# Optimization experiments

Hardware: AMD Instinct MI355X
Metric: run time of the kernel (lower is better)

## Reference

```python
import jax, jax.numpy as jnp
import numpy as np

B, N, L, H, D, IN = 512, 128, 10, 16, 8, 16
NT = B * N
E = NT * 16

def _lin(key, fan_in, shape):
    b = 1.0 / np.sqrt(fan_in)
    return jax.random.uniform(key, shape, jnp.float32, -b, b)

def setup_inputs() -> dict:
    key = jax.random.key(0)
    ks = jax.random.split(key, 12)
    x = jax.random.normal(ks[0], (NT, IN), jnp.float32)
    # within-graph random edges so to_dense_adj is well defined
    g = jax.random.randint(ks[1], (E,), 0, B)
    i = jax.random.randint(ks[2], (E,), 0, N)
    j = jax.random.randint(ks[3], (E,), 0, N)
    edge_index = jnp.stack([g * N + i, g * N + j]).astype(jnp.int32)
    return dict(
        x=x,
        gin_w1=_lin(ks[4], H, (2, L, H, H)),   # [ld/ud, layer, H, H]
        gin_b1=_lin(ks[5], H, (2, L, H)),
        gin_w2=_lin(ks[6], H, (2, L, H, H)),
        gin_b2=_lin(ks[7], H, (2, L, H)),
        mean_w=_lin(ks[8], H, (2, H, D)),
        mean_b=jnp.zeros((2, D), jnp.float32),
        std_w=_lin(ks[9], H, (2, H, D)),
        std_b=jnp.zeros((2, D), jnp.float32),
        edge_index=edge_index,
    )

def _encoder(x, w1, b1, w2, b2, mw, mb, sw, sb, src, dst):
    # PyG GIN stack: GINConv(MLP[Lin->ReLU->Lin]), eps=0, sum aggregation,
    # ReLU between layers (dropout = identity in eval mode).
    h = x
    for l in range(L):
        agg = jax.ops.segment_sum(h[src], dst, num_segments=NT)
        t = h + agg  # (1+eps)*x + sum_{j in N(i)} x_j with eps=0
        t = jnp.maximum(t @ w1[l] + b1[l], 0.0) @ w2[l] + b2[l]
        h = jnp.maximum(t, 0.0) if l < L - 1 else t
    mean = h @ mw + mb
    std = jax.nn.softplus(h @ sw + sb)
    return mean, std

def reference(x, gin_w1, gin_b1, gin_w2, gin_b2, mean_w, mean_b, std_w, std_b, edge_index):
    src, dst = edge_index[0], edge_index[1]
    enc = jax.vmap(_encoder, in_axes=(None, 0, 0, 0, 0, 0, 0, 0, 0, None, None))
    mean, std = enc(x, gin_w1, gin_b1, gin_w2, gin_b2,
                    mean_w, mean_b, std_w, std_b, src, dst)  # [2, NT, D]
    # reparameterized sample: eps ~ N(0,1) (prior.sample, detached)
    eps = jax.random.normal(jax.random.key(42), (2, NT, D), jnp.float32)
    z = mean + std * eps
    z_ld = z[0].reshape(B, N, D)
    z_ud = z[1].reshape(B, N, D)
    logits = jnp.einsum('bnd,bmd->bnm', z_ld, z_ud)  # per-graph inner-product decode
    dense_adj = jnp.zeros((B, N, N), jnp.float32).at[src // N, src % N, dst % N].add(1.0)
    n_pos = dense_adj.sum()
    posw = (B * N * N - n_pos) / n_pos
    # BCE-with-logits, pos_weight, reduction='sum'
    nll = jnp.sum(posw * dense_adj * jax.nn.softplus(-logits)
                  + (1.0 - dense_adj) * jax.nn.softplus(logits))
    # KL(N(mean,std) || N(0,1)), summed over both encoders
    kl = jnp.sum(-jnp.log(std) + 0.5 * (std * std + mean * mean) - 0.5)
    return nll, kl, jax.nn.sigmoid(logits), dense_adj
```

## Files before the change

kernel.cpp:

```cpp
#include <hip/hip_runtime.h>

#define B_    512
#define N_    128
#define L_    10
#define H_    16
#define D_    8
#define NT_   65536
#define E_    1048576
#define NNB_  8388608
#define CAP_  4096
#define CCAP_ 2816
#define HS_   20

__device__ __forceinline__ unsigned rotl32(unsigned v, int r){ return (v<<r)|(v>>(32-r)); }

__device__ __forceinline__ void threefry2x32(unsigned c0, unsigned c1, unsigned &o0, unsigned &o1){
  const unsigned ks0 = 0u, ks1 = 42u, ks2 = 0u ^ 42u ^ 0x1BD11BDAu;
  unsigned x0 = c0 + ks0, x1 = c1 + ks1;
#define TFR(r) { x0 += x1; x1 = rotl32(x1, r); x1 ^= x0; }
  TFR(13) TFR(15) TFR(26) TFR(6)   x0 += ks1; x1 += ks2 + 1u;
  TFR(17) TFR(29) TFR(16) TFR(24)  x0 += ks2; x1 += ks0 + 2u;
  TFR(13) TFR(15) TFR(26) TFR(6)   x0 += ks0; x1 += ks1 + 3u;
  TFR(17) TFR(29) TFR(16) TFR(24)  x0 += ks1; x1 += ks2 + 4u;
  TFR(13) TFR(15) TFR(26) TFR(6)   x0 += ks2; x1 += ks0 + 5u;
#undef TFR
  o0 = x0; o1 = x1;
}

__device__ __forceinline__ float erfinv_f(float x){
  float w = -log1pf(-x*x);
  float p;
  if (w < 5.0f) {
    w -= 2.5f;
    p = 2.81022636e-08f;
    p = fmaf(p, w, 3.43273939e-07f);
    p = fmaf(p, w, -3.5233877e-06f);
    p = fmaf(p, w, -4.39150654e-06f);
    p = fmaf(p, w, 0.00021858087f);
    p = fmaf(p, w, -0.00125372503f);
    p = fmaf(p, w, -0.00417768164f);
    p = fmaf(p, w, 0.246640727f);
    p = fmaf(p, w, 1.50140941f);
  } else {
    w = sqrtf(w) - 3.0f;
    p = -0.000200214257f;
    p = fmaf(p, w, 0.000100950558f);
    p = fmaf(p, w, 0.00134934322f);
    p = fmaf(p, w, -0.00367342844f);
    p = fmaf(p, w, 0.00573950773f);
    p = fmaf(p, w, -0.0076224613f);
    p = fmaf(p, w, 0.00943887047f);
    p = fmaf(p, w, 1.00167406f);
    p = fmaf(p, w, 2.83297682f);
  }
  return p * x;
}

__device__ __forceinline__ float softplus_f(float x){
  return fmaxf(x, 0.0f) + log1pf(expf(-fabsf(x)));
}

__device__ __forceinline__ void blockReduceAdd(double v, double* target){
  __shared__ double red[4];
  int lane = threadIdx.x & 63;
  int w    = threadIdx.x >> 6;
  #pragma unroll
  for(int off = 32; off > 0; off >>= 1) v += __shfl_down(v, off);
  if(lane == 0) red[w] = v;
  __syncthreads();
  if(threadIdx.x == 0){
    double s = red[0];
    int nw = (blockDim.x + 63) >> 6;
    for(int k = 1; k < nw; k++) s += red[k];
    atomicAdd(target, s);
  }
}

__global__ __launch_bounds__(256)
void k_bin(const int* __restrict__ ei, int* __restrict__ gcount,
           unsigned short* __restrict__ ebuf){
  __shared__ int cnt[512];
  __shared__ int gb[512];
  const int t = threadIdx.x;
  cnt[t] = 0; cnt[t + 256] = 0;
  __syncthreads();
  int kv[8];
  const int base = blockIdx.x * 2048;
  #pragma unroll
  for(int q = 0; q < 8; q++){
    int e = base + q*256 + t;
    int s = ei[e];
    int d = ei[E_ + e];
    int g = d >> 7;
    kv[q] = (g << 14) | ((s & 127) << 7) | (d & 127);
    atomicAdd(&cnt[g], 1);
  }
  __syncthreads();
  #pragma unroll
  for(int g = 0; g < 512; g += 256){
    int c = cnt[g + t];
    gb[g + t] = c ? atomicAdd(&gcount[g + t], c) : 0;
    cnt[g + t] = 0;
  }
  __syncthreads();
  #pragma unroll
  for(int q = 0; q < 8; q++){
    int g = kv[q] >> 14;
    int pos = atomicAdd(&cnt[g], 1);
    int idx = gb[g] + pos;
    if(idx < CAP_) ebuf[(size_t)g*CAP_ + idx] = (unsigned short)(kv[q] & 0x3FFF);
  }
}

__global__ __launch_bounds__(128)
void k_csr(const unsigned short* __restrict__ ebuf, const int* __restrict__ gcount,
           unsigned short* __restrict__ gcol, int* __restrict__ grow){
  __shared__ int cnt[128], off[128], sc[128];
  const int b = blockIdx.x, t = threadIdx.x;
  int ec = gcount[b]; if(ec > CAP_) ec = CAP_;
  const unsigned short* eb = ebuf + (size_t)b*CAP_;
  cnt[t] = 0;
  __syncthreads();
  for(int q = t; q < ec; q += 128) atomicAdd(&cnt[eb[q] & 127], 1);
  __syncthreads();
  int pdeg = (cnt[t] + 3) & ~3;
  sc[t] = pdeg;
  __syncthreads();
  for(int o = 1; o < 128; o <<= 1){
    int v = (t >= o) ? sc[t - o] : 0;
    __syncthreads();
    sc[t] += v;
    __syncthreads();
  }
  off[t] = sc[t] - pdeg;
  grow[b*129 + t] = off[t];
  if(t == 127) grow[b*129 + 128] = sc[127];
  cnt[t] = 0;
  __syncthreads();
  {
    uint4 s128; s128.x = s128.y = s128.z = s128.w = 0x00800080u;
    uint4* g4 = (uint4*)(gcol + (size_t)b*CCAP_);
    #pragma unroll
    for(int k = 0; k < 3; k++){ int q = t + 128*k; if(q < CCAP_/8) g4[q] = s128; }
  }
  __syncthreads();
  for(int q = t; q < ec; q += 128){
    int pk = eb[q];
    int d = pk & 127;
    int pos = atomicAdd(&cnt[d], 1);
    int idx = off[d] + pos;
    if(idx < CCAP_) gcol[(size_t)b*CCAP_ + idx] = (unsigned short)(pk >> 7);
  }
}

__global__ __launch_bounds__(128, 4)
void k_mega(const float* __restrict__ x, const unsigned short* __restrict__ gcol,
            const int* __restrict__ grow,
            const float* __restrict__ gw1, const float* __restrict__ gb1,
            const float* __restrict__ gw2, const float* __restrict__ gb2,
            const float* __restrict__ mw,  const float* __restrict__ mb,
            const float* __restrict__ sw,  const float* __restrict__ sb,
            float* __restrict__ z, double* acc){
  __shared__ __align__(16) float hh[129*HS_ + 4];
  __shared__ __align__(16) unsigned short col_l[CCAP_];
  const int b = blockIdx.x, e = blockIdx.y, t = threadIdx.x;

  {
    const float4* x4 = (const float4*)x + (size_t)b*512;
    #pragma unroll
    for(int k = 0; k < 4; k++){
      int q = t + 128*k;
      float4 v = x4[q];
      *(float4*)&hh[(q >> 2)*HS_ + (q & 3)*4] = v;
    }
    if(t < 16) hh[128*HS_ + t] = 0.0f;
  }
  {
    const uint4* gc4 = (const uint4*)(gcol + (size_t)b*CCAP_);
    uint4* cl4 = (uint4*)col_l;
    #pragma unroll
    for(int k = 0; k < 3; k++){ int q = t + 128*k; if(q < CCAP_/8) cl4[q] = gc4[q]; }
  }
  const int r0 = grow[b*129 + t], r1 = grow[b*129 + t + 1];
  __syncthreads();

  const float* w1g = gw1 + e*(L_*256);
  const float* w2g = gw2 + e*(L_*256);
  const float* b1g = gb1 + e*(L_*16);
  const float* b2g = gb2 + e*(L_*16);

  for(int l = 0; l < L_; l++){
    float ag[16];
    {
      const float4* hp = (const float4*)&hh[t*HS_];
      float4 s0 = hp[0], s1 = hp[1], s2 = hp[2], s3 = hp[3];
      ag[0]=s0.x; ag[1]=s0.y; ag[2]=s0.z; ag[3]=s0.w;
      ag[4]=s1.x; ag[5]=s1.y; ag[6]=s1.z; ag[7]=s1.w;
      ag[8]=s2.x; ag[9]=s2.y; ag[10]=s2.z; ag[11]=s2.w;
      ag[12]=s3.x; ag[13]=s3.y; ag[14]=s3.z; ag[15]=s3.w;
    }
    for(int r = r0; r < r1; r += 4){
      ushort4 c4 = *(const ushort4*)&col_l[r];
      const float4* n0 = (const float4*)&hh[c4.x*HS_];
      const float4* n1 = (const float4*)&hh[c4.y*HS_];
      const float4* n2 = (const float4*)&hh[c4.z*HS_];
      const float4* n3 = (const float4*)&hh[c4.w*HS_];
      #pragma unroll
      for(int c = 0; c < 4; c++){
        float4 v0 = n0[c], v1 = n1[c], v2 = n2[c], v3 = n3[c];
        ag[c*4+0] += v0.x + v1.x + v2.x + v3.x;
        ag[c*4+1] += v0.y + v1.y + v2.y + v3.y;
        ag[c*4+2] += v0.z + v1.z + v2.z + v3.z;
        ag[c*4+3] += v0.w + v1.w + v2.w + v3.w;
      }
    }
    float u[16];
    #pragma unroll
    for(int j = 0; j < 16; j++){
      float s = b1g[l*16 + j];
      #pragma unroll
      for(int k = 0; k < 16; k++) s = fmaf(ag[k], w1g[l*256 + k*16 + j], s);
      u[j] = fmaxf(s, 0.0f);
    }
    float ov[16];
    #pragma unroll
    for(int c = 0; c < 16; c++){
      float s = b2g[l*16 + c];
      #pragma unroll
      for(int k = 0; k < 16; k++) s = fmaf(u[k], w2g[l*256 + k*16 + c], s);
      ov[c] = (l < L_-1) ? fmaxf(s, 0.0f) : s;
    }
    __syncthreads();
    {
      float4* hw = (float4*)&hh[t*HS_];
      hw[0] = make_float4(ov[0], ov[1], ov[2], ov[3]);
      hw[1] = make_float4(ov[4], ov[5], ov[6], ov[7]);
      hw[2] = make_float4(ov[8], ov[9], ov[10], ov[11]);
      hw[3] = make_float4(ov[12], ov[13], ov[14], ov[15]);
    }
    __syncthreads();
  }

  float hv[16];
  {
    const float4* hp = (const float4*)&hh[t*HS_];
    float4 a0 = hp[0], a1 = hp[1], a2 = hp[2], a3 = hp[3];
    hv[0]=a0.x; hv[1]=a0.y; hv[2]=a0.z; hv[3]=a0.w;
    hv[4]=a1.x; hv[5]=a1.y; hv[6]=a1.z; hv[7]=a1.w;
    hv[8]=a2.x; hv[9]=a2.y; hv[10]=a2.z; hv[11]=a2.w;
    hv[12]=a3.x; hv[13]=a3.y; hv[14]=a3.z; hv[15]=a3.w;
  }
  const float* mwg = mw + e*128; const float* mbg = mb + e*8;
  const float* swg = sw + e*128; const float* sbg = sb + e*8;
  double kll = 0.0;
  float zv[8];
  unsigned fbase = ((unsigned)e*NT_ + (unsigned)(b*128 + t))*8u;
  #pragma unroll
  for(int d = 0; d < 8; d++){
    float mm = mbg[d], ss = sbg[d];
    #pragma unroll
    for(int k = 0; k < 16; k++){
      mm = fmaf(hv[k], mwg[k*8 + d], mm);
      ss = fmaf(hv[k], swg[k*8 + d], ss);
    }
    float stdv = softplus_f(ss);
    unsigned o0, o1; threefry2x32(0u, fbase + d, o0, o1);
    unsigned bits = o0 ^ o1;
    float uu = __uint_as_float((bits >> 9) | 0x3f800000u) - 1.0f;
    const float lo = -0.99999994f;
    float uval = fmaxf(lo, fmaf(uu, 2.0f, lo));
    float eps = 1.41421356f * erfinv_f(uval);
    zv[d] = mm + stdv * eps;
    float stdc = fmaxf(stdv, 1e-37f);
    float term = 0.5f*(stdv*stdv + mm*mm) - logf(stdc) - 0.5f;
    if(!(term == term) || term > 1e30f) term = 1e30f;
    kll += (double)term;
  }
  {
    float4* zp = (float4*)(z + (size_t)fbase);
    zp[0] = make_float4(zv[0], zv[1], zv[2], zv[3]);
    zp[1] = make_float4(zv[4], zv[5], zv[6], zv[7]);
  }
  blockReduceAdd(kll, acc + 1);
}

#define TSB_ 132
__global__ __launch_bounds__(256, 4)
void k_decode(const float* __restrict__ z, const unsigned short* __restrict__ ebuf,
              const int* __restrict__ gcount, float* __restrict__ sig,
              float* __restrict__ adj, double* acc){
  __shared__ float zl[1024];
  __shared__ float zu[1152];
  __shared__ unsigned tile32[128*TSB_/4];
  const int b = blockIdx.x, t = threadIdx.x;
  const float* zld = z + (size_t)b*1024;
  const float* zud = z + (size_t)NT_*8 + (size_t)b*1024;
  for(int k = t; k < 1024; k += 256){
    zl[k] = zld[k];
    zu[(k >> 3)*9 + (k & 7)] = zud[k];
  }
  {
    uint4 zz; zz.x = zz.y = zz.z = zz.w = 0u;
    uint4* t4 = (uint4*)tile32;
    for(int k = t; k < 128*TSB_/16; k += 256) t4[k] = zz;
  }
  __syncthreads();
  {
    int ec = gcount[b]; if(ec > CAP_) ec = CAP_;
    const unsigned short* eb = ebuf + (size_t)b*CAP_;
    for(int q = t; q < ec; q += 256){
      int pk = eb[q];
      int cell = (pk >> 7)*TSB_ + (pk & 127);
      atomicAdd(&tile32[cell >> 2], 1u << ((cell & 3)*8));
    }
  }
  __syncthreads();
  double local = 0.0;
  float* sigb = sig + (size_t)b*16384;
  float* adjb = adj + (size_t)b*16384;
  for(int it = 0; it < 16; it++){
    int base = it*1024 + t*4;
    int n = base >> 7, mcol = base & 127;
    const float* za = &zl[n*8];
    float xs[4];
    #pragma unroll
    for(int c = 0; c < 4; c++){
      const float* zb = &zu[(mcol + c)*9];
      float xx = 0.0f;
      #pragma unroll
      for(int d = 0; d < 8; d++) xx = fmaf(za[d], zb[d], xx);
      xs[c] = xx;
    }
    unsigned packed = tile32[(n*TSB_ + mcol) >> 2];
    float4 av;
    av.x = (float)( packed        & 0xFF);
    av.y = (float)((packed >> 8)  & 0xFF);
    av.z = (float)((packed >> 16) & 0xFF);
    av.w = (float)((packed >> 24) & 0xFF);
    float ads[4] = {av.x, av.y, av.z, av.w};
    float sgs[4];
    #pragma unroll
    for(int c = 0; c < 4; c++){
      float xx = xs[c];
      sgs[c] = 1.0f / (1.0f + expf(-xx));
      float cc  = log1pf(expf(-fabsf(xx)));
      float spp = fmaxf(xx, 0.0f) + cc;
      float spn = fmaxf(-xx, 0.0f) + cc;
      local += (double)(7.0f*ads[c]*spn + (1.0f - ads[c])*spp);
    }
    ((float4*)(sigb + base))[0] = make_float4(sgs[0], sgs[1], sgs[2], sgs[3]);
    ((float4*)(adjb + base))[0] = av;
  }
  blockReduceAdd(local, acc + 0);
}

__device__ __forceinline__ float clamp_finite(double v){
  if(v != v) return 0.0f;
  if(v >  3.3e38) return  3.3e38f;
  if(v < -3.3e38) return -3.3e38f;
  return (float)v;
}
__global__ void k_final(const double* __restrict__ acc, float* __restrict__ out){
  if(threadIdx.x == 0){
    out[0] = clamp_finite(acc[0]);
    out[1] = clamp_finite(acc[1]);
  }
}

extern "C" void kernel_launch(void* const* d_in, const int* in_sizes, int n_in,
                              void* d_out, int out_size, void* d_ws, size_t ws_size,
                              hipStream_t stream){
  const float* x   = (const float*)d_in[0];
  const float* gw1 = (const float*)d_in[1];
  const float* gb1 = (const float*)d_in[2];
  const float* gw2 = (const float*)d_in[3];
  const float* gb2 = (const float*)d_in[4];
  const float* mw  = (const float*)d_in[5];
  const float* mb  = (const float*)d_in[6];
  const float* sw  = (const float*)d_in[7];
  const float* sb  = (const float*)d_in[8];
  const int*   ei  = (const int*)d_in[9];

  float* out = (float*)d_out;
  float* sig = out + 2;
  float* adj = out + 2 + NNB_;

  char* ws = (char*)d_ws;
  int*            gcount = (int*)(ws);
  double*         acc    = (double*)(ws + 2048);
  unsigned short* ebuf   = (unsigned short*)(ws + 4096);
  unsigned short* gcol   = (unsigned short*)(ws + 4096 + 2*512*CAP_);
  int*            grow   = (int*)(ws + 4096 + 2*512*CAP_ + 2*512*CCAP_);
  float*          z      = (float*)(ws + 4096 + 2*512*CAP_ + 2*512*CCAP_ + 4*512*132);

  hipMemsetAsync(ws, 0, 4096, stream);

  k_bin   <<<E_/2048, 256, 0, stream>>>(ei, gcount, ebuf);
  k_csr   <<<B_, 128, 0, stream>>>(ebuf, gcount, gcol, grow);
  k_mega  <<<dim3(B_, 2), 128, 0, stream>>>(x, gcol, grow, gw1, gb1, gw2, gb2,
                                            mw, mb, sw, sb, z, acc);
  k_decode<<<B_, 256, 0, stream>>>(z, ebuf, gcount, sig, adj, acc);
  k_final <<<1, 64, 0, stream>>>(acc, out);
}
```

Measured before the change: 236.5 us.

## Fuse CSR build into GIN kernel and split features across 4 threads per node

Removes the separate k_csr kernel and builds the per-graph CSR directly in shared memory inside k_mega, which drops one launch and the global round trip through gcol/grow. k_mega now runs 512 threads per block, with four threads per node. Each thread handles a quarter of the hidden features for aggregation and the MLPs, exchanging them through new shared buffers agg_l and u_l. The aim is more parallelism and latency hiding per graph. The cost is extra barriers and shared-memory traffic per layer, and the CSR build is now done twice, once for each encoder block.

After: 233.6 us. No clear change (-1.2%).

```diff
diff --git a/kernel.cpp b/kernel.cpp
--- a/kernel.cpp
+++ b/kernel.cpp
@@ -61,7 +61,7 @@
 }
 
 __device__ __forceinline__ void blockReduceAdd(double v, double* target){
-  __shared__ double red[4];
+  __shared__ double red[8];
   int lane = threadIdx.x & 63;
   int w    = threadIdx.x >> 6;
   #pragma unroll
@@ -112,77 +112,68 @@
   }
 }
 
-__global__ __launch_bounds__(128)
-void k_csr(const unsigned short* __restrict__ ebuf, const int* __restrict__ gcount,
-           unsigned short* __restrict__ gcol, int* __restrict__ grow){
-  __shared__ int cnt[128], off[128], sc[128];
-  const int b = blockIdx.x, t = threadIdx.x;
-  int ec = gcount[b]; if(ec > CAP_) ec = CAP_;
-  const unsigned short* eb = ebuf + (size_t)b*CAP_;
-  cnt[t] = 0;
-  __syncthreads();
-  for(int q = t; q < ec; q += 128) atomicAdd(&cnt[eb[q] & 127], 1);
-  __syncthreads();
-  int pdeg = (cnt[t] + 3) & ~3;
-  sc[t] = pdeg;
-  __syncthreads();
-  for(int o = 1; o < 128; o <<= 1){
-    int v = (t >= o) ? sc[t - o] : 0;
-    __syncthreads();
-    sc[t] += v;
-    __syncthreads();
-  }
-  off[t] = sc[t] - pdeg;
-  grow[b*129 + t] = off[t];
-  if(t == 127) grow[b*129 + 128] = sc[127];
-  cnt[t] = 0;
-  __syncthreads();
-  {
-    uint4 s128; s128.x = s128.y = s128.z = s128.w = 0x00800080u;
-    uint4* g4 = (uint4*)(gcol + (size_t)b*CCAP_);
-    #pragma unroll
-    for(int k = 0; k < 3; k++){ int q = t + 128*k; if(q < CCAP_/8) g4[q] = s128; }
-  }
-  __syncthreads();
-  for(int q = t; q < ec; q += 128){
-    int pk = eb[q];
-    int d = pk & 127;
-    int pos = atomicAdd(&cnt[d], 1);
-    int idx = off[d] + pos;
-    if(idx < CCAP_) gcol[(size_t)b*CCAP_ + idx] = (unsigned short)(pk >> 7);
-  }
-}
-
-__global__ __launch_bounds__(128, 4)
-void k_mega(const float* __restrict__ x, const unsigned short* __restrict__ gcol,
-            const int* __restrict__ grow,
+__global__ __launch_bounds__(512, 8)
+void k_mega(const float* __restrict__ x, const unsigned short* __restrict__ ebuf,
+            const int* __restrict__ gcount,
             const float* __restrict__ gw1, const float* __restrict__ gb1,
             const float* __restrict__ gw2, const float* __restrict__ gb2,
             const float* __restrict__ mw,  const float* __restrict__ mb,
             const float* __restrict__ sw,  const float* __restrict__ sb,
             float* __restrict__ z, double* acc){
   __shared__ __align__(16) float hh[129*HS_ + 4];
+  __shared__ __align__(16) float agg_l[128*HS_];
+  __shared__ __align__(16) float u_l[128*HS_];
   __shared__ __align__(16) unsigned short col_l[CCAP_];
+  __shared__ int cnt[128];
+  __shared__ int sc[128];
+  __shared__ int off_l[129];
+
   const int b = blockIdx.x, e = blockIdx.y, t = threadIdx.x;
+  const int lane = t & 63;
+  const int q  = __builtin_amdgcn_readfirstlane((t >> 6) & 3);
+  const int q4 = q * 4;
+  const int n  = lane + ((t >> 8) << 6);
 
   {
     const float4* x4 = (const float4*)x + (size_t)b*512;
-    #pragma unroll
-    for(int k = 0; k < 4; k++){
-      int q = t + 128*k;
-      float4 v = x4[q];
-      *(float4*)&hh[(q >> 2)*HS_ + (q & 3)*4] = v;
-    }
+    float4 v = x4[t];
+    *(float4*)&hh[(t >> 2)*HS_ + (t & 3)*4] = v;
     if(t < 16) hh[128*HS_ + t] = 0.0f;
-  }
+    if(t < 128) cnt[t] = 0;
+  }
+  __syncthreads();
+
+  int ec = gcount[b]; if(ec > CAP_) ec = CAP_;
+  const unsigned short* eb = ebuf + (size_t)b*CAP_;
+  for(int i = t; i < ec; i += 512) atomicAdd(&cnt[eb[i] & 127], 1);
+  __syncthreads();
+  int pdeg = 0;
+  if(t < 128){ pdeg = (cnt[t] + 3) & ~3; sc[t] = pdeg; }
+  __syncthreads();
+  for(int o = 1; o < 128; o <<= 1){
+    int v = 0;
+    if(t < 128 && t >= o) v = sc[t - o];
+    __syncthreads();
+    if(t < 128) sc[t] += v;
+    __syncthreads();
+  }
+  if(t < 128){ off_l[t] = sc[t] - pdeg; cnt[t] = 0; }
+  if(t == 127) off_l[128] = sc[127];
   {
-    const uint4* gc4 = (const uint4*)(gcol + (size_t)b*CCAP_);
-    uint4* cl4 = (uint4*)col_l;
-    #pragma unroll
-    for(int k = 0; k < 3; k++){ int q = t + 128*k; if(q < CCAP_/8) cl4[q] = gc4[q]; }
-  }
-  const int r0 = grow[b*129 + t], r1 = grow[b*129 + t + 1];
-  __syncthreads();
+    uint4 s128; s128.x = s128.y = s128.z = s128.w = 0x00800080u;
+    uint4* c4 = (uint4*)col_l;
+    if(t < CCAP_/8) c4[t] = s128;
+  }
+  __syncthreads();
+  for(int i = t; i < ec; i += 512){
+    int pk = eb[i];
+    int d = pk & 127;
+    int pos = atomicAdd(&cnt[d], 1);
+    int idx = off_l[d] + pos;
+    if(idx < CCAP_) col_l[idx] = (unsigned short)(pk >> 7);
+  }
+  __syncthreads();
+  const int r0 = off_l[n], r1 = off_l[n + 1];
 
   const float* w1g = gw1 + e*(L_*256);
   const float* w2g = gw2 + e*(L_*256);
@@ -190,60 +181,87 @@
   const float* b2g = gb2 + e*(L_*16);
 
   for(int l = 0; l < L_; l++){
-    float ag[16];
+    float ag0, ag1, ag2, ag3;
     {
-      const float4* hp = (const float4*)&hh[t*HS_];
-      float4 s0 = hp[0], s1 = hp[1], s2 = hp[2], s3 = hp[3];
-      ag[0]=s0.x; ag[1]=s0.y; ag[2]=s0.z; ag[3]=s0.w;
-      ag[4]=s1.x; ag[5]=s1.y; ag[6]=s1.z; ag[7]=s1.w;
-      ag[8]=s2.x; ag[9]=s2.y; ag[10]=s2.z; ag[11]=s2.w;
-      ag[12]=s3.x; ag[13]=s3.y; ag[14]=s3.z; ag[15]=s3.w;
+      float4 s = *(const float4*)&hh[n*HS_ + q4];
+      ag0 = s.x; ag1 = s.y; ag2 = s.z; ag3 = s.w;
     }
     for(int r = r0; r < r1; r += 4){
       ushort4 c4 = *(const ushort4*)&col_l[r];
-      const float4* n0 = (const float4*)&hh[c4.x*HS_];
-      const float4* n1 = (const float4*)&hh[c4.y*HS_];
-      const float4* n2 = (const float4*)&hh[c4.z*HS_];
-      const float4* n3 = (const float4*)&hh[c4.w*HS_];
-      #pragma unroll
-      for(int c = 0; c < 4; c++){
-        float4 v0 = n0[c], v1 = n1[c], v2 = n2[c], v3 = n3[c];
-        ag[c*4+0] += v0.x + v1.x + v2.x + v3.x;
-        ag[c*4+1] += v0.y + v1.y + v2.y + v3.y;
-        ag[c*4+2] += v0.z + v1.z + v2.z + v3.z;
-        ag[c*4+3] += v0.w + v1.w + v2.w + v3.w;
-      }
-    }
-    float u[16];
+      float4 v0 = *(const float4*)&hh[c4.x*HS_ + q4];
+      float4 v1 = *(const float4*)&hh[c4.y*HS_ + q4];
+      float4 v2 = *(const float4*)&hh[c4.z*HS_ + q4];
+      float4 v3 = *(const float4*)&hh[c4.w*HS_ + q4];
+      ag0 += v0.x + v1.x + v2.x + v3.x;
+      ag1 += v0.y + v1.y + v2.y + v3.y;
+      ag2 += v0.z + v1.z + v2.z + v3.z;
+      ag3 += v0.w + v1.w + v2.w + v3.w;
+    }
+    *(float4*)&agg_l[n*HS_ + q4] = make_float4(ag0, ag1, ag2, ag3);
+    __syncthreads();
+
+    float av[16];
+    {
+      const float4* ap = (const float4*)&agg_l[n*HS_];
+      float4 a0 = ap[0], a1 = ap[1], a2 = ap[2], a3 = ap[3];
+      av[0]=a0.x; av[1]=a0.y; av[2]=a0.z; av[3]=a0.w;
+      av[4]=a1.x; av[5]=a1.y; av[6]=a1.z; av[7]=a1.w;
+      av[8]=a2.x; av[9]=a2.y; av[10]=a2.z; av[11]=a2.w;
+      av[12]=a3.x; av[13]=a3.y; av[14]=a3.z; av[15]=a3.w;
+    }
+    const float* w1c = w1g + l*256 + q4;
+    float u0 = b1g[l*16 + q4 + 0];
+    float u1 = b1g[l*16 + q4 + 1];
+    float u2 = b1g[l*16 + q4 + 2];
+    float u3 = b1g[l*16 + q4 + 3];
     #pragma unroll
-    for(int j = 0; j < 16; j++){
-      float s = b1g[l*16 + j];
-      #pragma unroll
-      for(int k = 0; k < 16; k++) s = fmaf(ag[k], w1g[l*256 + k*16 + j], s);
-      u[j] = fmaxf(s, 0.0f);
-    }
-    float ov[16];
+    for(int k = 0; k < 16; k++){
+      float a = av[k];
+      const float* wr = w1c + k*16;
+      u0 = fmaf(a, wr[0], u0);
+      u1 = fmaf(a, wr[1], u1);
+      u2 = fmaf(a, wr[2], u2);
+      u3 = fmaf(a, wr[3], u3);
+    }
+    u0 = fmaxf(u0, 0.0f); u1 = fmaxf(u1, 0.0f);
+    u2 = fmaxf(u2, 0.0f); u3 = fmaxf(u3, 0.0f);
+    *(float4*)&u_l[n*HS_ + q4] = make_float4(u0, u1, u2, u3);
+    __syncthreads();
+
+    float uv[16];
+    {
+      const float4* up = (const float4*)&u_l[n*HS_];
+      float4 a0 = up[0], a1 = up[1], a2 = up[2], a3 = up[3];
+      uv[0]=a0.x; uv[1]=a0.y; uv[2]=a0.z; uv[3]=a0.w;
+      uv[4]=a1.x; uv[5]=a1.y; uv[6]=a1.z; uv[7]=a1.w;
+      uv[8]=a2.x; uv[9]=a2.y; uv[10]=a2.z; uv[11]=a2.w;
+      uv[12]=a3.x; uv[13]=a3.y; uv[14]=a3.z; uv[15]=a3.w;
+    }
+    const float* w2c = w2g + l*256 + q4;
+    float o0 = b2g[l*16 + q4 + 0];
+    float o1 = b2g[l*16 + q4 + 1];
+    float o2 = b2g[l*16 + q4 + 2];
+    float o3 = b2g[l*16 + q4 + 3];
     #pragma unroll
-    for(int c = 0; c < 16; c++){
-      float s = b2g[l*16 + c];
-      #pragma unroll
-      for(int k = 0; k < 16; k++) s = fmaf(u[k], w2g[l*256 + k*16 + c], s);
-      ov[c] = (l < L_-1) ? fmaxf(s, 0.0f) : s;
-    }
-    __syncthreads();
-    {
-      float4* hw = (float4*)&hh[t*HS_];
-      hw[0] = make_float4(ov[0], ov[1], ov[2], ov[3]);
-      hw[1] = make_float4(ov[4], ov[5], ov[6], ov[7]);
-      hw[2] = make_float4(ov[8], ov[9], ov[10], ov[11]);
-      hw[3] = make_float4(ov[12], ov[13], ov[14], ov[15]);
-    }
+    for(int k = 0; k < 16; k++){
+      float a = uv[k];
+      const float* wr = w2c + k*16;
+      o0 = fmaf(a, wr[0], o0);
+      o1 = fmaf(a, wr[1], o1);
+      o2 = fmaf(a, wr[2], o2);
+      o3 = fmaf(a, wr[3], o3);
+    }
+    if(l < L_ - 1){
+      o0 = fmaxf(o0, 0.0f); o1 = fmaxf(o1, 0.0f);
+      o2 = fmaxf(o2, 0.0f); o3 = fmaxf(o3, 0.0f);
+    }
+    *(float4*)&hh[n*HS_ + q4] = make_float4(o0, o1, o2, o3);
     __syncthreads();
   }
 
   float hv[16];
   {
-    const float4* hp = (const float4*)&hh[t*HS_];
+    const float4* hp = (const float4*)&hh[n*HS_];
     float4 a0 = hp[0], a1 = hp[1], a2 = hp[2], a3 = hp[3];
     hv[0]=a0.x; hv[1]=a0.y; hv[2]=a0.z; hv[3]=a0.w;
     hv[4]=a1.x; hv[5]=a1.y; hv[6]=a1.z; hv[7]=a1.w;
@@ -253,10 +271,11 @@
   const float* mwg = mw + e*128; const float* mbg = mb + e*8;
   const float* swg = sw + e*128; const float* sbg = sb + e*8;
   double kll = 0.0;
-  float zv[8];
-  unsigned fbase = ((unsigned)e*NT_ + (unsigned)(b*128 + t))*8u;
+  float zv[2];
+  unsigned nodeBase = ((unsigned)e*NT_ + (unsigned)(b*128 + n))*8u;
   #pragma unroll
-  for(int d = 0; d < 8; d++){
+  for(int dd = 0; dd < 2; dd++){
+    int d = q*2 + dd;
     float mm = mbg[d], ss = sbg[d];
     #pragma unroll
     for(int k = 0; k < 16; k++){
@@ -264,23 +283,19 @@
       ss = fmaf(hv[k], swg[k*8 + d], ss);
     }
     float stdv = softplus_f(ss);
-    unsigned o0, o1; threefry2x32(0u, fbase + d, o0, o1);
+    unsigned o0, o1; threefry2x32(0u, nodeBase + (unsigned)d, o0, o1);
     unsigned bits = o0 ^ o1;
     float uu = __uint_as_float((bits >> 9) | 0x3f800000u) - 1.0f;
     const float lo = -0.99999994f;
     float uval = fmaxf(lo, fmaf(uu, 2.0f, lo));
     float eps = 1.41421356f * erfinv_f(uval);
-    zv[d] = mm + stdv * eps;
+    zv[dd] = mm + stdv * eps;
     float stdc = fmaxf(stdv, 1e-37f);
     float term = 0.5f*(stdv*stdv + mm*mm) - logf(stdc) - 0.5f;
     if(!(term == term) || term > 1e30f) term = 1e30f;
     kll += (double)term;
   }
-  {
-    float4* zp = (float4*)(z + (size_t)fbase);
-    zp[0] = make_float4(zv[0], zv[1], zv[2], zv[3]);
-    zp[1] = make_float4(zv[4], zv[5], zv[6], zv[7]);
-  }
+  *(float2*)&z[nodeBase + (unsigned)(q*2)] = make_float2(zv[0], zv[1]);
   blockReduceAdd(kll, acc + 1);
 }
 
@@ -389,15 +404,12 @@
   int*            gcount = (int*)(ws);
   double*         acc    = (double*)(ws + 2048);
   unsigned short* ebuf   = (unsigned short*)(ws + 4096);
-  unsigned short* gcol   = (unsigned short*)(ws + 4096 + 2*512*CAP_);
-  int*            grow   = (int*)(ws + 4096 + 2*512*CAP_ + 2*512*CCAP_);
-  float*          z      = (float*)(ws + 4096 + 2*512*CAP_ + 2*512*CCAP_ + 4*512*132);
+  float*          z      = (float*)(ws + 4096 + 2*512*CAP_);
 
   hipMemsetAsync(ws, 0, 4096, stream);
 
   k_bin   <<<E_/2048, 256, 0, stream>>>(ei, gcount, ebuf);
-  k_csr   <<<B_, 128, 0, stream>>>(ebuf, gcount, gcol, grow);
-  k_mega  <<<dim3(B_, 2), 128, 0, stream>>>(x, gcol, grow, gw1, gb1, gw2, gb2,
+  k_mega  <<<dim3(B_, 2), 512, 0, stream>>>(x, ebuf, gcount, gw1, gb1, gw2, gb2,
                                             mw, mb, sw, sb, z, acc);
   k_decode<<<B_, 256, 0, stream>>>(z, ebuf, gcount, sig, adj, acc);
   k_final <<<1, 64, 0, stream>>>(acc, out);
```
